# Kernel optimization log

Hardware: AMD Instinct MI355X
Metric: run time of the kernel (lower is better)

The kernel has to match this reference:

```python
import jax, jax.numpy as jnp
import numpy as np
from jax import lax

N = 2_097_152  # grid length
WENO5_MULT_BIAS = 0.1


def _conv1d(x, w, b, pad):
    # x: [1, C_in, L], w: [C_out, C_in, K] -> [1, C_out, L]
    y = lax.conv_general_dilated(x, w, window_strides=(1,), padding=[(pad, pad)],
                                 dimension_numbers=('NCH', 'OIH', 'NCH'))
    return y + b[None, :, None]


def _inner_nn_weno5(dif, w1, b1, w2, b2, w3, b3, w4, b4, w5, b5, w6, b6):
    # dif: [N] -> multiplier signal [N] in (0,1) via sigmoid
    x = dif[None, None, :]
    x = jax.nn.elu(_conv1d(x, w1, b1, 2))
    x = jax.nn.elu(_conv1d(x, w2, b2, 2))
    x = jax.nn.elu(_conv1d(x, w3, b3, 0))
    x = jax.nn.elu(_conv1d(x, w4, b4, 0))
    x = jax.nn.elu(_conv1d(x, w5, b5, 1))
    x = jax.nn.sigmoid(_conv1d(x, w6, b6, 0))
    return x[0, 0, :]


def _avg_diff(uu):
    # centered average of forward differences, replicated at the edges -> [N]
    dif = uu[1:] - uu[:-1]
    dif_left = jnp.concatenate([dif, dif[-1:]])
    dif_right = jnp.concatenate([dif[:1], dif])
    return 0.5 * dif_left + 0.5 * dif_right


def _fluxes_minus(u):
    f0 = (11 * u[3:-2] - 7 * u[4:-1] + 2 * u[5:]) / 6
    f1 = (2 * u[2:-3] + 5 * u[3:-2] - u[4:-1]) / 6
    f2 = (-u[1:-4] + 5 * u[2:-3] + 2 * u[3:-2]) / 6
    return f0, f1, f2


def _betas_minus(u):
    b0 = 13 / 12 * (u[3:-2] - 2 * u[4:-1] + u[5:]) ** 2 + 1 / 4 * (3 * u[3:-2] - 4 * u[4:-1] + u[5:]) ** 2
    b1 = 13 / 12 * (u[2:-3] - 2 * u[3:-2] + u[4:-1]) ** 2 + 1 / 4 * (u[2:-3] - u[4:-1]) ** 2
    b2 = 13 / 12 * (u[1:-4] - 2 * u[2:-3] + u[3:-2]) ** 2 + 1 / 4 * (u[1:-4] - 4 * u[2:-3] + 3 * u[3:-2]) ** 2
    return b0, b1, b2


def _weno5(uu, e, beta_mult):
    # w5_minus=True, mweno=True, mapped=False, trainable=True branch
    ur = uu[1:]
    ul = uu[:-1]
    fp = _fluxes_minus(ur)
    fn = _fluxes_minus(ul)
    bp = _betas_minus(ur)
    bn = _betas_minus(ul)
    # multipliers bm[3+shift:-3+shift] for shift in {-1,0,1}
    mul = (beta_mult[2:-4], beta_mult[3:-3], beta_mult[4:-2])
    bp = [b * m for b, m in zip(bp, mul)]
    bn = [b * m for b, m in zip(bn, mul)]
    ds = (1 / 10, 6 / 10, 3 / 10)

    def omegas_mweno(bs):
        brs = (bs[2] - bs[0]) ** 2
        o = [d / (e + b) ** 2 * (brs + (e + b) ** 2) for b, d in zip(bs, ds)]
        s = o[0] + o[1] + o[2]
        return [x / s for x in o]

    op = omegas_mweno(bp)
    on = omegas_mweno(bn)
    fluxp = op[0] * fp[0] + op[1] * fp[1] + op[2] * fp[2]
    fluxn = on[0] * fn[0] + on[1] * fn[1] + on[2] * fn[2]
    return fluxp - fluxn  # [N-6]


def setup_inputs() -> dict:
    key = jax.random.key(0)
    ks = jax.random.split(key, 14)
    uu = jax.random.normal(ks[0], (N,), dtype=jnp.float32)
    e = jnp.float32(1e-6)
    s = 0.1  # weight scale for stability
    w1 = s * jax.random.normal(ks[1], (20, 1, 5), jnp.float32)
    b1 = s * jax.random.normal(ks[2], (20,), jnp.float32)
    w2 = s * jax.random.normal(ks[3], (40, 20, 5), jnp.float32)
    b2 = s * jax.random.normal(ks[4], (40,), jnp.float32)
    w3 = s * jax.random.normal(ks[5], (80, 40, 1), jnp.float32)
    b3 = s * jax.random.normal(ks[6], (80,), jnp.float32)
    w4 = s * jax.random.normal(ks[7], (40, 80, 1), jnp.float32)
    b4 = s * jax.random.normal(ks[8], (40,), jnp.float32)
    w5 = s * jax.random.normal(ks[9], (20, 40, 3), jnp.float32)
    b5 = s * jax.random.normal(ks[10], (20,), jnp.float32)
    w6 = s * jax.random.normal(ks[11], (1, 20, 1), jnp.float32)
    b6 = s * jax.random.normal(ks[12], (1,), jnp.float32)
    return {"uu": uu, "e": e, "w1": w1, "b1": b1, "w2": w2, "b2": b2,
            "w3": w3, "b3": b3, "w4": w4, "b4": b4, "w5": w5, "b5": b5,
            "w6": w6, "b6": b6}


def reference(uu, e, w1, b1, w2, b2, w3, b3, w4, b4, w5, b5, w6, b6):
    dif = _avg_diff(uu)
    beta_mult = _inner_nn_weno5(dif, w1, b1, w2, b2, w3, b3, w4, b4, w5, b5, w6, b6) + WENO5_MULT_BIAS
    return _weno5(uu, e, beta_mult)
```

## Files before the change

### kernel.cpp

```cpp
#include <hip/hip_runtime.h>
#include <math.h>

#define NTHREADS 256
#define TOUT 118
#define NP 120
#define WROWS 30
#define X1S 40
#define T3S 88
#define NDIF 128
#define NDIFP 144
#define NUU 130
#define WREG (WROWS * T3S)
#define LOG2E 1.44269504f
#define LN2   0.69314718f

#define F2_BASE 0
#define F3_BASE 15
#define F4_BASE 25
#define F5_BASE 34
#define F1_BASE 42
#define NFRAGS 44

typedef unsigned short u16;
typedef unsigned int u32;
typedef __attribute__((ext_vector_type(8))) short bf16x8;
typedef __attribute__((ext_vector_type(4))) float f32x4;

__device__ __forceinline__ float exp2_f(float x) {
#if __has_builtin(__builtin_amdgcn_exp2f)
    return __builtin_amdgcn_exp2f(x);
#else
    float r; asm("v_exp_f32 %0, %1" : "=v"(r) : "v"(x)); return r;
#endif
}
__device__ __forceinline__ float eluc_f(float y) {
    float t = exp2_f(fminf(y, 0.0f));
    return fmaxf(y, fmaf(t, LOG2E, -LOG2E));
}
__device__ __forceinline__ float rcp_f(float x) {
    return __builtin_amdgcn_rcpf(x);
}
__device__ __forceinline__ float sq_f(float x) { return x * x; }
__device__ __forceinline__ u16 f2bf(float f) {
    union { float f; u32 u; } v; v.f = f;
    u32 r = v.u + 0x7FFFu + ((v.u >> 16) & 1u);
    return (u16)(r >> 16);
}
__device__ __forceinline__ u32 pack_trunc(float a, float b) {
    union { float f; u32 u; } va, vb; va.f = a; vb.f = b;
#if __has_builtin(__builtin_amdgcn_perm)
    return __builtin_amdgcn_perm(vb.u, va.u, 0x07060302u);
#else
    return (vb.u & 0xFFFF0000u) | (va.u >> 16);
#endif
}
__device__ __forceinline__ u32 pack_rne(float a, float b) {
    return (u32)f2bf(a) | ((u32)f2bf(b) << 16);
}

__global__ __launch_bounds__(64) void build_frags_kernel(
    const float* __restrict__ w1, const float* __restrict__ w2,
    const float* __restrict__ w3, const float* __restrict__ w4,
    const float* __restrict__ w5, u16* __restrict__ ws)
{
    const int f = blockIdx.x;
    const int lane = threadIdx.x;
    const int m = lane & 15;
    const int q = lane >> 4;
    float wvv[8];
    #pragma unroll
    for (int j = 0; j < 8; ++j) wvv[j] = 0.0f;

    if (f < F3_BASE) {
        int mt = (f - F2_BASE) / 5, s = (f - F2_BASE) % 5;
        int oc = mt * 16 + m;
        #pragma unroll
        for (int j = 0; j < 8; ++j) {
            int ic = q * 8 + j;
            if (oc < 40 && ic < 20) wvv[j] = w2[oc * 100 + ic * 5 + s];
        }
    } else if (f < F4_BASE) {
        int mt = (f - F3_BASE) / 2, s = (f - F3_BASE) % 2;
        int oc = mt * 16 + m;
        #pragma unroll
        for (int j = 0; j < 8; ++j) {
            int k = s * 32 + q * 8 + j;
            if (k < 40) wvv[j] = w3[oc * 40 + k];
        }
    } else if (f < F5_BASE) {
        int mt = (f - F4_BASE) / 3, s = (f - F4_BASE) % 3;
        int oc = mt * 16 + m;
        #pragma unroll
        for (int j = 0; j < 8; ++j) {
            int k = s * 32 + q * 8 + j;
            if (oc < 40 && k < 80) wvv[j] = w4[oc * 80 + k];
        }
    } else if (f < F1_BASE) {
        int mt = (f - F5_BASE) / 4, s = (f - F5_BASE) % 4;
        int oc = mt * 16 + m;
        int k0 = s * 32 + q * 8;
        int dk = k0 / 40, ic0 = k0 - dk * 40;
        #pragma unroll
        for (int j = 0; j < 8; ++j) {
            if (oc < 20 && k0 < 120) wvv[j] = w5[oc * 120 + (ic0 + j) * 3 + dk];
        }
    } else {
        int mt = f - F1_BASE;
        int oc = mt * 16 + m;
        #pragma unroll
        for (int j = 0; j < 8; ++j) {
            int k = q * 8 + j;
            if (oc < 20 && k < 5) wvv[j] = w1[oc * 5 + k] * LOG2E;
        }
    }
    u32 pk[4];
    #pragma unroll
    for (int p = 0; p < 4; ++p)
        pk[p] = (u32)f2bf(wvv[2 * p]) | ((u32)f2bf(wvv[2 * p + 1]) << 16);
    u32* wp = (u32*)&ws[(f * 64 + lane) * 8];
    wp[0] = pk[0]; wp[1] = pk[1]; wp[2] = pk[2]; wp[3] = pk[3];
}

__device__ __forceinline__ bf16x8 ld_frag(const u16* ws, int f, int lane) {
    return *(const bf16x8*)&ws[(f * 64 + lane) * 8];
}

__global__ __launch_bounds__(NTHREADS, 2) void weno_nn_kernel(
    const float* __restrict__ uu, const float* __restrict__ e_ptr,
    const float* __restrict__ w1, const float* __restrict__ b1,
    const float* __restrict__ b2, const float* __restrict__ b3,
    const float* __restrict__ b4, const float* __restrict__ b5,
    const float* __restrict__ w6, const float* __restrict__ b6,
    const u16* __restrict__ wfr,
    float* __restrict__ out, int n_out, int N)
{
    __shared__ float s_uu[NUU];
    __shared__ u32 s_difh[NDIFP];
    __shared__ __align__(16) u16 bufA[4 * WREG];
    __shared__ __align__(16) u16 bufB[(NP + 2) * 40];

    float* s_beta = (float*)s_difh;

    const int tid  = threadIdx.x;
    const int lane = tid & 63;
    const int wv_id = __builtin_amdgcn_readfirstlane(tid >> 6);
    const int m    = lane & 15;
    const int q    = lane >> 4;
    const int J0   = blockIdx.x * TOUT;
    const int P0   = J0 + 2;
    const int U0   = J0 - 4;

    u16* xw = &bufA[wv_id * WREG];

    for (int i = tid; i < NUU; i += NTHREADS) {
        int g = U0 + i;
        s_uu[i] = (g >= 0 && g < N) ? uu[g] : 0.0f;
    }
    __syncthreads();

    {
        auto difval = [&](int d) -> float {
            if (d >= NDIF) return 0.0f;
            int g = P0 - 5 + d;
            if (g < 0 || g >= N) return 0.0f;
            int j1 = g < N - 2 ? g : N - 2;
            int j0 = g - 1 > 0 ? g - 1 : 0;
            float dl = s_uu[j1 + 1 - U0] - s_uu[j1 - U0];
            float dr = s_uu[j0 + 1 - U0] - s_uu[j0 - U0];
            return 0.5f * (dl + dr);
        };
        for (int d = tid; d < NDIFP; d += NTHREADS)
            s_difh[d] = pack_rne(difval(d), difval(d + 1));
    }
    __syncthreads();


    {
        bf16x8 a1[2];
        a1[0] = ld_frag(wfr, F1_BASE + 0, lane);
        a1[1] = ld_frag(wfr, F1_BASE + 1, lane);
        f32x4 bias1[2];
        #pragma unroll
        for (int r = 0; r < 4; ++r) {
            bias1[0][r] = b1[4 * q + r] * LOG2E;
            int oc = 16 + 4 * q + r;
            bias1[1][r] = (oc < 20) ? b1[oc] * LOG2E : 0.0f;
        }
        #pragma unroll
        for (int it = 0; it < 3; ++it) {
            const int li = it * 16 + m;
            const int pos = wv_id * WROWS + li;
            bf16x8 bfrag;
            u32* bw = (u32*)&bfrag;
            bw[0] = s_difh[pos];
            bw[1] = s_difh[pos + 2];
            bw[2] = s_difh[pos + 4];
            bw[3] = 0;
            f32x4 acc0 = bias1[0];
            f32x4 acc1 = bias1[1];
            acc0 = __builtin_amdgcn_mfma_f32_16x16x32_bf16(a1[0], bfrag, acc0, 0, 0, 0);
            acc1 = __builtin_amdgcn_mfma_f32_16x16x32_bf16(a1[1], bfrag, acc1, 0, 0, 0);
            if (li < WROWS + 4) {
                int g = P0 - 3 + pos;
                bool valid = (g >= 0 && g < N);
                float e0 = valid ? eluc_f(acc0[0]) : 0.0f;
                float e1 = valid ? eluc_f(acc0[1]) : 0.0f;
                float e2 = valid ? eluc_f(acc0[2]) : 0.0f;
                float e3 = valid ? eluc_f(acc0[3]) : 0.0f;
                u32* wp = (u32*)&xw[li * X1S + 4 * q];
                wp[0] = pack_trunc(e0, e1);
                wp[1] = pack_trunc(e2, e3);
                if (q == 0) {
                    float f0 = valid ? eluc_f(acc1[0]) : 0.0f;
                    float f1 = valid ? eluc_f(acc1[1]) : 0.0f;
                    float f2 = valid ? eluc_f(acc1[2]) : 0.0f;
                    float f3 = valid ? eluc_f(acc1[3]) : 0.0f;
                    u32* wp2 = (u32*)&xw[li * X1S + 16];
                    wp2[0] = pack_trunc(f0, f1);
                    wp2[1] = pack_trunc(f2, f3);
                } else {
                    u32* wpz = (u32*)&xw[li * X1S + 20 + (q - 1) * 4];
                    wpz[0] = 0; wpz[1] = 0;
                }
            }
        }
    }
    __builtin_amdgcn_sched_barrier(0);

    {
        bf16x8 a2[3][5];
        #pragma unroll
        for (int mt = 0; mt < 3; ++mt)
            #pragma unroll
            for (int s = 0; s < 5; ++s)
                a2[mt][s] = ld_frag(wfr, F2_BASE + mt * 5 + s, lane);
        f32x4 bias2[3];
        #pragma unroll
        for (int mt = 0; mt < 3; ++mt) {
            #pragma unroll
            for (int r = 0; r < 4; ++r) {
                int oc = mt * 16 + 4 * q + r;
                bias2[mt][r] = (oc < 40) ? b2[oc] * LOG2E : 0.0f;
            }
        }
        for (int t = 0; t < 2; ++t) {
            const int lr = t * 16 + m;
            const int gr = wv_id * WROWS + lr;
            f32x4 acc[3];
            #pragma unroll
            for (int mt = 0; mt < 3; ++mt) acc[mt] = bias2[mt];
            #pragma unroll
            for (int s = 0; s < 5; ++s) {
                bf16x8 bfrag = *(const bf16x8*)&xw[(lr + s) * X1S + q * 8];
                #pragma unroll
                for (int mt = 0; mt < 3; ++mt)
                    acc[mt] = __builtin_amdgcn_mfma_f32_16x16x32_bf16(a2[mt][s], bfrag, acc[mt], 0, 0, 0);
            }
            #pragma unroll
            for (int mt = 0; mt < 3; ++mt) {
                int oc0 = mt * 16 + 4 * q;
                if (lr < WROWS && oc0 < 40) {
                    u32* wp = (u32*)&bufB[gr * 40 + oc0];
                    wp[0] = pack_trunc(eluc_f(acc[mt][0]), eluc_f(acc[mt][1]));
                    wp[1] = pack_trunc(eluc_f(acc[mt][2]), eluc_f(acc[mt][3]));
                }
            }
        }
    }
    __builtin_amdgcn_sched_barrier(0);

    {
        bf16x8 a3[5][2];
        #pragma unroll
        for (int mt = 0; mt < 5; ++mt)
            #pragma unroll
            for (int s = 0; s < 2; ++s)
                a3[mt][s] = ld_frag(wfr, F3_BASE + mt * 2 + s, lane);
        f32x4 bias3[5];
        #pragma unroll
        for (int mt = 0; mt < 5; ++mt) {
            #pragma unroll
            for (int r = 0; r < 4; ++r) bias3[mt][r] = b3[mt * 16 + 4 * q + r] * LOG2E;
        }
        for (int t = 0; t < 2; ++t) {
            const int lr = t * 16 + m;
            const int gr = wv_id * WROWS + lr;
            f32x4 acc[5];
            #pragma unroll
            for (int mt = 0; mt < 5; ++mt) acc[mt] = bias3[mt];
            {
                bf16x8 bfrag = *(const bf16x8*)&bufB[gr * 40 + q * 8];
                #pragma unroll
                for (int mt = 0; mt < 5; ++mt)
                    acc[mt] = __builtin_amdgcn_mfma_f32_16x16x32_bf16(a3[mt][0], bfrag, acc[mt], 0, 0, 0);
            }
            {
                bf16x8 bfrag = *(const bf16x8*)&bufB[gr * 40 + ((q == 0) ? 32 : 0)];
                #pragma unroll
                for (int mt = 0; mt < 5; ++mt)
                    acc[mt] = __builtin_amdgcn_mfma_f32_16x16x32_bf16(a3[mt][1], bfrag, acc[mt], 0, 0, 0);
            }
            #pragma unroll
            for (int mt = 0; mt < 5; ++mt) {
                int oc0 = mt * 16 + 4 * q;
                if (lr < WROWS) {
                    u32* wp = (u32*)&xw[lr * T3S + oc0];
                    wp[0] = pack_trunc(eluc_f(acc[mt][0]), eluc_f(acc[mt][1]));
                    wp[1] = pack_trunc(eluc_f(acc[mt][2]), eluc_f(acc[mt][3]));
                }
            }
        }
    }
    __builtin_amdgcn_sched_barrier(0);

    {
        bf16x8 a4[3][3];
        #pragma unroll
        for (int mt = 0; mt < 3; ++mt)
            #pragma unroll
            for (int s = 0; s < 3; ++s)
                a4[mt][s] = ld_frag(wfr, F4_BASE + mt * 3 + s, lane);
        f32x4 bias4[3];
        #pragma unroll
        for (int mt = 0; mt < 3; ++mt) {
            #pragma unroll
            for (int r = 0; r < 4; ++r) {
                int oc = mt * 16 + 4 * q + r;
                bias4[mt][r] = (oc < 40) ? b4[oc] * LOG2E : 0.0f;
            }
        }
        if (tid < 80) bufB[NP * 40 + tid] = 0;
        for (int t = 0; t < 2; ++t) {
            const int lr = t * 16 + m;
            const int gr = wv_id * WROWS + lr;
            f32x4 acc[3];
            #pragma unroll
            for (int mt = 0; mt < 3; ++mt) acc[mt] = bias4[mt];
            #pragma unroll
            for (int s = 0; s < 3; ++s) {
                int k0 = s * 32 + q * 8;
                bf16x8 bfrag = *(const bf16x8*)&xw[lr * T3S + ((k0 < 80) ? k0 : 0)];
                #pragma unroll
                for (int mt = 0; mt < 3; ++mt)
                    acc[mt] = __builtin_amdgcn_mfma_f32_16x16x32_bf16(a4[mt][s], bfrag, acc[mt], 0, 0, 0);
            }
            #pragma unroll
            for (int mt = 0; mt < 3; ++mt) {
                int oc0 = mt * 16 + 4 * q;
                if (lr < WROWS && oc0 < 40) {
                    u32* wp = (u32*)&bufB[gr * 40 + oc0];
                    wp[0] = pack_trunc(eluc_f(acc[mt][0]), eluc_f(acc[mt][1]));
                    wp[1] = pack_trunc(eluc_f(acc[mt][2]), eluc_f(acc[mt][3]));
                }
            }
        }
    }
    __syncthreads();

    {
        bf16x8 a5[2][4];
        #pragma unroll
        for (int mt = 0; mt < 2; ++mt)
            #pragma unroll
            for (int s = 0; s < 4; ++s)
                a5[mt][s] = ld_frag(wfr, F5_BASE + mt * 4 + s, lane);
        f32x4 bias5[2];
        #pragma unroll
        for (int mt = 0; mt < 2; ++mt) {
            #pragma unroll
            for (int r = 0; r < 4; ++r) {
                int oc = mt * 16 + 4 * q + r;
                bias5[mt][r] = (oc < 20) ? b5[oc] * LOG2E : 0.0f;
            }
        }
        float w6a[4], w6b[4];
        #pragma unroll
        for (int r = 0; r < 4; ++r) {
            w6a[r] = w6[4 * q + r] * LN2;
            w6b[r] = (q == 0) ? w6[16 + r] * LN2 : 0.0f;
        }
        const float b6v = b6[0];

        for (int t = 0; t < 2; ++t) {
            const int N0 = (wv_id * 2 + t) * 16;
            const int row = N0 + m;
            f32x4 acc[2];
            #pragma unroll
            for (int mt = 0; mt < 2; ++mt) acc[mt] = bias5[mt];
            #pragma unroll
            for (int s = 0; s < 4; ++s) {
                int k0 = s * 32 + q * 8;
                int dk = (k0 < 120) ? (k0 / 40) : 0;
                int ic0 = (k0 < 120) ? (k0 - dk * 40) : 0;
                int rr = row + dk;
                rr = (rr < NP + 2) ? rr : (NP + 1);
                bf16x8 bfrag = *(const bf16x8*)&bufB[rr * 40 + ic0];
                #pragma unroll
                for (int mt = 0; mt < 2; ++mt)
                    acc[mt] = __builtin_amdgcn_mfma_f32_16x16x32_bf16(a5[mt][s], bfrag, acc[mt], 0, 0, 0);
            }
            float p = 0.0f;
            #pragma unroll
            for (int r = 0; r < 4; ++r) p += w6a[r] * eluc_f(acc[0][r]);
            #pragma unroll
            for (int r = 0; r < 4; ++r) p += w6b[r] * eluc_f(acc[1][r]);
            p += __shfl_xor(p, 16);
            p += __shfl_xor(p, 32);
            float aa = p + b6v;
            if (q == 0 && row < NP)
                s_beta[row] = rcp_f(1.0f + __expf(-aa)) + 0.1f;
        }
    }
    __syncthreads();

    const float eps = e_ptr[0];
    if (tid < TOUT) {
        int j = J0 + tid;
        if (j < n_out) {
            float a  = s_uu[tid + 5];
            float b  = s_uu[tid + 6];
            float c  = s_uu[tid + 7];
            float d  = s_uu[tid + 8];
            float ee = s_uu[tid + 9];
            float f  = s_uu[tid + 10];
            float m0 = s_beta[tid];
            float m1 = s_beta[tid + 1];
            float m2 = s_beta[tid + 2];

            const float i6 = 1.0f / 6.0f;
            float fp0 = (11.f * d - 7.f * ee + 2.f * f) * i6;
            float fp1 = (2.f * c + 5.f * d - ee) * i6;
            float fp2 = (-b + 5.f * c + 2.f * d) * i6;
            float fn0 = (11.f * c - 7.f * d + 2.f * ee) * i6;
            float fn1 = (2.f * b + 5.f * c - d) * i6;
            float fn2 = (-a + 5.f * b + 2.f * c) * i6;

            const float c1312 = 13.f / 12.f;
            float bp0 = c1312 * sq_f(d - 2.f * ee + f) + 0.25f * sq_f(3.f * d - 4.f * ee + f);
            float bp1 = c1312 * sq_f(c - 2.f * d + ee) + 0.25f * sq_f(c - ee);
            float bp2 = c1312 * sq_f(b - 2.f * c + d) + 0.25f * sq_f(b - 4.f * c + 3.f * d);
            float bn0 = c1312 * sq_f(c - 2.f * d + ee) + 0.25f * sq_f(3.f * c - 4.f * d + ee);
            float bn1 = c1312 * sq_f(b - 2.f * c + d) + 0.25f * sq_f(b - d);
            float bn2 = c1312 * sq_f(a - 2.f * b + c) + 0.25f * sq_f(a - 4.f * b + 3.f * c);

            bp0 *= m0; bp1 *= m1; bp2 *= m2;
            bn0 *= m0; bn1 *= m1; bn2 *= m2;

            float q0 = eps + bp0; q0 *= q0;
            float q1 = eps + bp1; q1 *= q1;
            float q2 = eps + bp2; q2 *= q2;
            float brs = bp2 - bp0; brs *= brs;
            float o0 = 0.1f * (1.f + brs * rcp_f(q0));
            float o1 = 0.6f * (1.f + brs * rcp_f(q1));
            float o2 = 0.3f * (1.f + brs * rcp_f(q2));
            float inv = rcp_f(o0 + o1 + o2);
            float fluxp = (o0 * fp0 + o1 * fp1 + o2 * fp2) * inv;

            q0 = eps + bn0; q0 *= q0;
            q1 = eps + bn1; q1 *= q1;
            q2 = eps + bn2; q2 *= q2;
            brs = bn2 - bn0; brs *= brs;
            o0 = 0.1f * (1.f + brs * rcp_f(q0));
            o1 = 0.6f * (1.f + brs * rcp_f(q1));
            o2 = 0.3f * (1.f + brs * rcp_f(q2));
            inv = rcp_f(o0 + o1 + o2);
            float fluxn = (o0 * fn0 + o1 * fn1 + o2 * fn2) * inv;

            out[j] = fluxp - fluxn;
        }
    }
}

extern "C" void kernel_launch(void* const* d_in, const int* in_sizes, int n_in,
                              void* d_out, int out_size, void* d_ws, size_t ws_size,
                              hipStream_t stream) {
    const float* uu = (const float*)d_in[0];
    const float* e  = (const float*)d_in[1];
    const float* w1 = (const float*)d_in[2];
    const float* b1 = (const float*)d_in[3];
    const float* w2 = (const float*)d_in[4];
    const float* b2 = (const float*)d_in[5];
    const float* w3 = (const float*)d_in[6];
    const float* b3 = (const float*)d_in[7];
    const float* w4 = (const float*)d_in[8];
    const float* b4 = (const float*)d_in[9];
    const float* w5 = (const float*)d_in[10];
    const float* b5 = (const float*)d_in[11];
    const float* w6 = (const float*)d_in[12];
    const float* b6 = (const float*)d_in[13];
    float* out = (float*)d_out;
    u16* wfr = (u16*)d_ws;
    const int N = in_sizes[0];
    const int nblocks = (out_size + TOUT - 1) / TOUT;

    build_frags_kernel<<<NFRAGS, 64, 0, stream>>>(w1, w2, w3, w4, w5, wfr);
    weno_nn_kernel<<<nblocks, NTHREADS, 0, stream>>>(
        uu, e, w1, b1, b2, b3, b4, b5, w6, b6, wfr,
        out, out_size, N);
}
```

Before: 295.5 us.

## Widen tile to 128 positions per block so MFMA row tiles are fully used

Raises the output tile from 118 to 126 positions, so each wave covers exactly 32 rows and the 16-row MFMA tiles carry no padding. This lets the row-bound guards and the clamp in the layer-5 read be dropped. It also folds the final sigmoid into exp2 by leaving the LN2 scaling off w6 and scaling b6 by LOG2E instead. The aim is fewer blocks and less wasted MFMA work per output. In exchange, shared memory per block grows (larger bufA and bufB), which may affect occupancy.

```diff
diff --git a/kernel.cpp b/kernel.cpp
--- a/kernel.cpp
+++ b/kernel.cpp
@@ -2,17 +2,15 @@
 #include <math.h>
 
 #define NTHREADS 256
-#define TOUT 118
-#define NP 120
-#define WROWS 30
+#define TOUT 126
+#define NP 128
 #define X1S 40
 #define T3S 88
-#define NDIF 128
-#define NDIFP 144
-#define NUU 130
-#define WREG (WROWS * T3S)
+#define NDIF 136
+#define NDIFP 148
+#define NUU 138
+#define WREG 2816
 #define LOG2E 1.44269504f
-#define LN2   0.69314718f
 
 #define F2_BASE 0
 #define F3_BASE 15
@@ -137,7 +135,7 @@
     __shared__ float s_uu[NUU];
     __shared__ u32 s_difh[NDIFP];
     __shared__ __align__(16) u16 bufA[4 * WREG];
-    __shared__ __align__(16) u16 bufB[(NP + 2) * 40];
+    __shared__ __align__(16) u16 bufB[130 * 40];
 
     float* s_beta = (float*)s_difh;
 
@@ -189,7 +187,7 @@
         #pragma unroll
         for (int it = 0; it < 3; ++it) {
             const int li = it * 16 + m;
-            const int pos = wv_id * WROWS + li;
+            const int pos = wv_id * 32 + li;
             bf16x8 bfrag;
             u32* bw = (u32*)&bfrag;
             bw[0] = s_difh[pos];
@@ -200,7 +198,7 @@
             f32x4 acc1 = bias1[1];
             acc0 = __builtin_amdgcn_mfma_f32_16x16x32_bf16(a1[0], bfrag, acc0, 0, 0, 0);
             acc1 = __builtin_amdgcn_mfma_f32_16x16x32_bf16(a1[1], bfrag, acc1, 0, 0, 0);
-            if (li < WROWS + 4) {
+            if (li < 36) {
                 int g = P0 - 3 + pos;
                 bool valid = (g >= 0 && g < N);
                 float e0 = valid ? eluc_f(acc0[0]) : 0.0f;
@@ -245,7 +243,7 @@
         }
         for (int t = 0; t < 2; ++t) {
             const int lr = t * 16 + m;
-            const int gr = wv_id * WROWS + lr;
+            const int gr = wv_id * 32 + lr;
             f32x4 acc[3];
             #pragma unroll
             for (int mt = 0; mt < 3; ++mt) acc[mt] = bias2[mt];
@@ -259,7 +257,7 @@
             #pragma unroll
             for (int mt = 0; mt < 3; ++mt) {
                 int oc0 = mt * 16 + 4 * q;
-                if (lr < WROWS && oc0 < 40) {
+                if (oc0 < 40) {
                     u32* wp = (u32*)&bufB[gr * 40 + oc0];
                     wp[0] = pack_trunc(eluc_f(acc[mt][0]), eluc_f(acc[mt][1]));
                     wp[1] = pack_trunc(eluc_f(acc[mt][2]), eluc_f(acc[mt][3]));
@@ -284,7 +282,7 @@
         }
         for (int t = 0; t < 2; ++t) {
             const int lr = t * 16 + m;
-            const int gr = wv_id * WROWS + lr;
+            const int gr = wv_id * 32 + lr;
             f32x4 acc[5];
             #pragma unroll
             for (int mt = 0; mt < 5; ++mt) acc[mt] = bias3[mt];
@@ -303,11 +301,9 @@
             #pragma unroll
             for (int mt = 0; mt < 5; ++mt) {
                 int oc0 = mt * 16 + 4 * q;
-                if (lr < WROWS) {
-                    u32* wp = (u32*)&xw[lr * T3S + oc0];
-                    wp[0] = pack_trunc(eluc_f(acc[mt][0]), eluc_f(acc[mt][1]));
-                    wp[1] = pack_trunc(eluc_f(acc[mt][2]), eluc_f(acc[mt][3]));
-                }
+                u32* wp = (u32*)&xw[lr * T3S + oc0];
+                wp[0] = pack_trunc(eluc_f(acc[mt][0]), eluc_f(acc[mt][1]));
+                wp[1] = pack_trunc(eluc_f(acc[mt][2]), eluc_f(acc[mt][3]));
             }
         }
     }
@@ -329,10 +325,10 @@
                 bias4[mt][r] = (oc < 40) ? b4[oc] * LOG2E : 0.0f;
             }
         }
-        if (tid < 80) bufB[NP * 40 + tid] = 0;
+        if (tid < 80) bufB[128 * 40 + tid] = 0;
         for (int t = 0; t < 2; ++t) {
             const int lr = t * 16 + m;
-            const int gr = wv_id * WROWS + lr;
+            const int gr = wv_id * 32 + lr;
             f32x4 acc[3];
             #pragma unroll
             for (int mt = 0; mt < 3; ++mt) acc[mt] = bias4[mt];
@@ -347,7 +343,7 @@
             #pragma unroll
             for (int mt = 0; mt < 3; ++mt) {
                 int oc0 = mt * 16 + 4 * q;
-                if (lr < WROWS && oc0 < 40) {
+                if (oc0 < 40) {
                     u32* wp = (u32*)&bufB[gr * 40 + oc0];
                     wp[0] = pack_trunc(eluc_f(acc[mt][0]), eluc_f(acc[mt][1]));
                     wp[1] = pack_trunc(eluc_f(acc[mt][2]), eluc_f(acc[mt][3]));
@@ -376,10 +372,10 @@
         float w6a[4], w6b[4];
         #pragma unroll
         for (int r = 0; r < 4; ++r) {
-            w6a[r] = w6[4 * q + r] * LN2;
-            w6b[r] = (q == 0) ? w6[16 + r] * LN2 : 0.0f;
-        }
-        const float b6v = b6[0];
+            w6a[r] = w6[4 * q + r];
+            w6b[r] = (q == 0) ? w6[16 + r] : 0.0f;
+        }
+        const float b6v = b6[0] * LOG2E;
 
         for (int t = 0; t < 2; ++t) {
             const int N0 = (wv_id * 2 + t) * 16;
@@ -392,9 +388,7 @@
                 int k0 = s * 32 + q * 8;
                 int dk = (k0 < 120) ? (k0 / 40) : 0;
                 int ic0 = (k0 < 120) ? (k0 - dk * 40) : 0;
-                int rr = row + dk;
-                rr = (rr < NP + 2) ? rr : (NP + 1);
-                bf16x8 bfrag = *(const bf16x8*)&bufB[rr * 40 + ic0];
+                bf16x8 bfrag = *(const bf16x8*)&bufB[(row + dk) * 40 + ic0];
                 #pragma unroll
                 for (int mt = 0; mt < 2; ++mt)
                     acc[mt] = __builtin_amdgcn_mfma_f32_16x16x32_bf16(a5[mt][s], bfrag, acc[mt], 0, 0, 0);
@@ -407,8 +401,8 @@
             p += __shfl_xor(p, 16);
             p += __shfl_xor(p, 32);
             float aa = p + b6v;
-            if (q == 0 && row < NP)
-                s_beta[row] = rcp_f(1.0f + __expf(-aa)) + 0.1f;
+            if (q == 0)
+                s_beta[row] = rcp_f(1.0f + exp2_f(-aa)) + 0.1f;
         }
     }
     __syncthreads();
```

New measurement: 280.0 us. -5.2%, faster.
